# Kernel tuning notes

Measured on AMD Instinct MI355X. Metric: run time of the kernel, lower is better.

The kernel has to match this reference:

```python
import jax, jax.numpy as jnp
import numpy as np

N_NODES = 50000
N_EDGES = 800000


def _sage_layer(h, src, dst, ew, Ws, Wn, b, activate):
    # DGL SAGEConv, aggregator_type='mean', with edge weights:
    # message m_e = ew_e * h_src ; neigh = mean over incoming edges (divide by in-degree)
    msg = h[src] * ew[:, None]                       # [E, F] irregular gather
    agg = jax.ops.segment_sum(msg, dst, num_segments=N_NODES)
    deg = jax.ops.segment_sum(jnp.ones_like(ew), dst, num_segments=N_NODES)
    h_neigh = agg / jnp.maximum(deg, 1.0)[:, None]   # zero for isolated nodes
    out = h @ Ws + h_neigh @ Wn + b                  # fc_self + fc_neigh + bias
    return jnp.tanh(out) if activate else out


def setup_inputs() -> dict:
    key = jax.random.key(0)
    ks = jax.random.split(key, 12)
    d = 64
    inp = {
        "b_z": jax.random.normal(ks[0], (N_NODES, d), dtype=jnp.float32),
        "edge_src": jax.random.randint(ks[1], (N_EDGES,), 0, N_NODES, dtype=jnp.int32),
        "edge_dst": jax.random.randint(ks[2], (N_EDGES,), 0, N_NODES, dtype=jnp.int32),
        "edge_weight": jax.random.uniform(ks[3], (N_EDGES,), dtype=jnp.float32),
        "Ws0": jax.random.normal(ks[4], (64, 32), dtype=jnp.float32) / np.sqrt(64),
        "Wn0": jax.random.normal(ks[5], (64, 32), dtype=jnp.float32) / np.sqrt(64),
        "b0": jnp.zeros((32,), jnp.float32),
        "Ws1": jax.random.normal(ks[6], (32, 16), dtype=jnp.float32) / np.sqrt(32),
        "Wn1": jax.random.normal(ks[7], (32, 16), dtype=jnp.float32) / np.sqrt(32),
        "b1": jnp.zeros((16,), jnp.float32),
        "Ws2": jax.random.normal(ks[8], (16, 1), dtype=jnp.float32) / np.sqrt(16),
        "Wn2": jax.random.normal(ks[9], (16, 1), dtype=jnp.float32) / np.sqrt(16),
        "b2": jnp.zeros((1,), jnp.float32),
        "b_size": 500,
    }
    return inp


def reference(b_z, edge_src, edge_dst, edge_weight,
              Ws0, Wn0, b0, Ws1, Wn1, b1, Ws2, Wn2, b2, b_size):
    h = _sage_layer(b_z, edge_src, edge_dst, edge_weight, Ws0, Wn0, b0, True)
    h = _sage_layer(h, edge_src, edge_dst, edge_weight, Ws1, Wn1, b1, True)
    h = _sage_layer(h, edge_src, edge_dst, edge_weight, Ws2, Wn2, b2, False)
    x_hat = h.reshape(b_size, -1)
    return x_hat
```

## Files before the change

### kernel.cpp

```cpp
#include <hip/hip_runtime.h>
#include <hip/hip_bf16.h>

#define N_NODES 50000
#define N_EDGES 800000
#define BLK 256
#define NRANGE 256
#define RNG 196
#define NPART 256
#define EPB 3125
#define PCAP 44
#define SCAP 48
#define GRID_F 2048

#define EW_SCALE (1.0f / 65535.0f)

__device__ inline void unpack8(uint4 g, float* f) {
    f[0] = __uint_as_float(g.x << 16); f[1] = __uint_as_float(g.x & 0xffff0000u);
    f[2] = __uint_as_float(g.y << 16); f[3] = __uint_as_float(g.y & 0xffff0000u);
    f[4] = __uint_as_float(g.z << 16); f[5] = __uint_as_float(g.z & 0xffff0000u);
    f[6] = __uint_as_float(g.w << 16); f[7] = __uint_as_float(g.w & 0xffff0000u);
}
__device__ inline void unpack4(uint2 g, float* f) {
    f[0] = __uint_as_float(g.x << 16); f[1] = __uint_as_float(g.x & 0xffff0000u);
    f[2] = __uint_as_float(g.y << 16); f[3] = __uint_as_float(g.y & 0xffff0000u);
}

__global__ void premul0_partA_kernel(const float* __restrict__ b_z,
                                     const int* __restrict__ src,
                                     const int* __restrict__ dst,
                                     const float* __restrict__ ew,
                                     const float* __restrict__ Wn0,
                                     const float* __restrict__ Ws0,
                                     const float* __restrict__ b0,
                                     __hip_bfloat16* __restrict__ hW0,
                                     float* __restrict__ hSelf0,
                                     uint2* __restrict__ lists,
                                     int* __restrict__ pcnt, int N) {
    __shared__ __align__(16) unsigned char SMEM[28080];
    int tid = threadIdx.x;
    int bid = blockIdx.x;

    if (bid < NPART) {
        uint2* sSorted = (uint2*)SMEM;
        int* hist = (int*)(SMEM + 25000);
        int* pfx  = (int*)(SMEM + 26024);
        int* cur  = (int*)(SMEM + 27048);
        int base = bid * EPB;
        hist[tid] = 0;
        __syncthreads();
        for (int i = tid; i < EPB; i += BLK)
            atomicAdd(&hist[dst[base + i] / RNG], 1);
        __syncthreads();
        {
            int v = hist[tid];
            pfx[tid] = v;
            __syncthreads();
            for (int off = 1; off < NRANGE; off <<= 1) {
                int t = (tid >= off) ? pfx[tid - off] : 0;
                __syncthreads();
                pfx[tid] += t;
                __syncthreads();
            }
            int incl = pfx[tid];
            __syncthreads();
            pfx[tid] = incl - v;
            cur[tid] = incl - v;
            __syncthreads();
        }
        for (int i = tid; i < EPB; i += BLK) {
            int e = base + i;
            int d = dst[e];
            unsigned int q = __float2uint_rn(ew[e] * 65535.0f);
            unsigned int py = (q << 16) | (unsigned int)src[e];
            int pos = atomicAdd(&cur[d / RNG], 1);
            sSorted[pos] = make_uint2(py, (unsigned int)d);
        }
        __syncthreads();
        for (int i = tid; i < EPB; i += BLK) {
            int lo = 0, hi = NRANGE - 1;
            while (lo < hi) { int mid = (lo + hi + 1) >> 1; if (pfx[mid] <= i) lo = mid; else hi = mid - 1; }
            int idx = i - pfx[lo];
            if (idx < PCAP)
                lists[((size_t)lo * NPART + bid) * PCAP + idx] = sSorted[i];
        }
        pcnt[tid * NPART + bid] = min(hist[tid], PCAP);
    } else {
        float* sWn = (float*)SMEM;
        float* sWs = (float*)(SMEM + 8192);
        float* sb  = (float*)(SMEM + 16384);
        float* sh  = (float*)(SMEM + 16512);
        for (int i = tid; i < 64 * 32; i += BLK) { sWn[i] = Wn0[i]; sWs[i] = Ws0[i]; }
        if (tid < 32) sb[tid] = b0[tid];
        const int nch = (N + 7) / 8;
        const int stride = GRID_F - NPART;
        int r = tid >> 5, j = tid & 31;
        for (int c = bid - NPART; c < nch; c += stride) {
            __syncthreads();
            int nodeBase = c * 8;
            for (int i = tid; i < 8 * 64; i += BLK) {
                int rr = i >> 6, k = i & 63;
                int n = nodeBase + rr;
                sh[rr * 65 + k] = (n < N) ? b_z[(size_t)n * 64 + k] : 0.f;
            }
            __syncthreads();
            int n = nodeBase + r;
            if (n < N) {
                float an = 0.f, as = 0.f;
#pragma unroll
                for (int k = 0; k < 64; ++k) {
                    float hk = sh[r * 65 + k];
                    an += hk * sWn[k * 32 + j];
                    as += hk * sWs[k * 32 + j];
                }
                hW0[(size_t)n * 32 + j] = __float2bfloat16(an);
                hSelf0[(size_t)n * 32 + j] = as + sb[j];
            }
        }
    }
}

__global__ void partB_kernel(const uint2* __restrict__ lists,
                             const int* __restrict__ pcnt,
                             unsigned int* __restrict__ bucket,
                             int* __restrict__ counts, int N) {
    __shared__ unsigned int lslot[RNG * SCAP];
    __shared__ int lcnt[RNG];
    __shared__ int scnt[NPART];
    __shared__ int spfx[NPART];
    int tid = threadIdx.x;
    int r = blockIdx.x;
    int node0 = r * RNG;
    int nn = min(RNG, N - node0);
    if (nn <= 0) return;

    for (int i = tid; i < RNG; i += BLK) lcnt[i] = 0;
    scnt[tid] = pcnt[r * NPART + tid];
    __syncthreads();
    {
        int v = scnt[tid];
        spfx[tid] = v;
        __syncthreads();
        for (int off = 1; off < NPART; off <<= 1) {
            int t = (tid >= off) ? spfx[tid - off] : 0;
            __syncthreads();
            spfx[tid] += t;
            __syncthreads();
        }
        int incl = spfx[tid];
        __syncthreads();
        spfx[tid] = incl - v;
        __syncthreads();
    }
    int T = spfx[NPART - 1] + scnt[NPART - 1];
    for (int j = tid; j < T; j += BLK) {
        int lo = 0, hi = NPART - 1;
        while (lo < hi) { int mid = (lo + hi + 1) >> 1; if (spfx[mid] <= j) lo = mid; else hi = mid - 1; }
        int idx = j - spfx[lo];
        uint2 en = lists[((size_t)r * NPART + lo) * PCAP + idx];
        int node = (int)en.y - node0;
        int pos = atomicAdd(&lcnt[node], 1);
        if (pos < SCAP) lslot[node * SCAP + pos] = en.x;
    }
    __syncthreads();
    unsigned int* __restrict__ gb = bucket + (size_t)node0 * SCAP;
    int tot = nn * SCAP;
    for (int i = tid; i < tot; i += BLK) gb[i] = lslot[i];
    for (int i = tid; i < nn; i += BLK) counts[node0 + i] = min(lcnt[i], SCAP);
}

__global__ void agg0_kernel(const __hip_bfloat16* __restrict__ hW0,
                            const float* __restrict__ hSelf0,
                            const int* __restrict__ cnts,
                            const unsigned int* __restrict__ bucket,
                            const float* __restrict__ Wn1,
                            const float* __restrict__ Ws1,
                            const float* __restrict__ b1,
                            __hip_bfloat16* __restrict__ hW1,
                            float* __restrict__ hSelf1, int N) {
    __shared__ float sWn[32 * 16];
    __shared__ float sWs[32 * 16];
    __shared__ float sb[16];
    __shared__ float sh2[64 * 33];
    int tid = threadIdx.x;
    for (int i = tid; i < 32 * 16; i += BLK) { sWn[i] = Wn1[i]; sWs[i] = Ws1[i]; }
    if (tid < 16) sb[tid] = b1[tid];

    const uint4* __restrict__ tab = (const uint4*)hW0;
    int nodeBase = blockIdx.x * 64;
    int r = tid >> 2;
    int l = tid & 3;
    int n = nodeBase + r;
    if (n < N) {
        int cnt = cnts[n];
        int cn  = min(cnt, SCAP);
        const unsigned int* __restrict__ ep = bucket + (size_t)n * SCAP;
        float acc[8];
#pragma unroll
        for (int t = 0; t < 8; ++t) acc[t] = 0.f;
        int k = 0;
        for (; k + 8 <= cn; k += 8) {
            uint4 ev0 = *(const uint4*)(ep + k);
            uint4 ev1 = *(const uint4*)(ep + k + 4);
            unsigned int ee[8] = { ev0.x, ev0.y, ev0.z, ev0.w,
                                   ev1.x, ev1.y, ev1.z, ev1.w };
            uint4 g[8];
            float w[8];
#pragma unroll
            for (int u = 0; u < 8; ++u) {
                g[u] = tab[(size_t)(ee[u] & 0xffffu) * 4 + l];
                w[u] = (float)(ee[u] >> 16) * EW_SCALE;
            }
#pragma unroll
            for (int u = 0; u < 8; ++u) {
                float f[8];
                unpack8(g[u], f);
#pragma unroll
                for (int t = 0; t < 8; ++t) acc[t] += w[u] * f[t];
            }
        }
        for (; k < cn; ++k) {
            unsigned int e = ep[k];
            float w = (float)(e >> 16) * EW_SCALE;
            uint4 g = tab[(size_t)(e & 0xffffu) * 4 + l];
            float f[8];
            unpack8(g, f);
#pragma unroll
            for (int t = 0; t < 8; ++t) acc[t] += w * f[t];
        }
        float invdeg = 1.0f / fmaxf((float)cnt, 1.0f);
        const float4* __restrict__ hs = (const float4*)(hSelf0 + (size_t)n * 32);
        float4 s0 = hs[l * 2], s1 = hs[l * 2 + 1];
        float sf[8] = { s0.x, s0.y, s0.z, s0.w, s1.x, s1.y, s1.z, s1.w };
#pragma unroll
        for (int t = 0; t < 8; ++t)
            sh2[r * 33 + l * 8 + t] = tanhf(acc[t] * invdeg + sf[t]);
    }
    __syncthreads();
    for (int idx = tid; idx < 64 * 16; idx += BLK) {
        int r2 = idx >> 4, j2 = idx & 15;
        int n2 = nodeBase + r2;
        if (n2 < N) {
            float an = 0.f, as = 0.f;
#pragma unroll
            for (int k = 0; k < 32; ++k) {
                float hk = sh2[r2 * 33 + k];
                an += hk * sWn[k * 16 + j2];
                as += hk * sWs[k * 16 + j2];
            }
            hW1[(size_t)n2 * 16 + j2] = __float2bfloat16(an);
            hSelf1[(size_t)n2 * 16 + j2] = as + sb[j2];
        }
    }
}

__global__ void agg1_kernel(const __hip_bfloat16* __restrict__ hW1,
                            const float* __restrict__ hSelf1,
                            const int* __restrict__ cnts,
                            const unsigned int* __restrict__ bucket,
                            const float* __restrict__ Wn2,
                            const float* __restrict__ Ws2,
                            const float* __restrict__ b2,
                            float* __restrict__ hWf,
                            float* __restrict__ hSelf2, int N) {
    int tid = threadIdx.x;
    int r = tid >> 2;
    int l = tid & 3;
    int n = blockIdx.x * 64 + r;
    if (n >= N) return;

    const uint2* __restrict__ tab = (const uint2*)hW1;
    int cnt = cnts[n];
    int cn  = min(cnt, SCAP);
    const unsigned int* __restrict__ ep = bucket + (size_t)n * SCAP;
    float acc[4];
#pragma unroll
    for (int t = 0; t < 4; ++t) acc[t] = 0.f;
    int k = 0;
    for (; k + 8 <= cn; k += 8) {
        uint4 ev0 = *(const uint4*)(ep + k);
        uint4 ev1 = *(const uint4*)(ep + k + 4);
        unsigned int ee[8] = { ev0.x, ev0.y, ev0.z, ev0.w,
                               ev1.x, ev1.y, ev1.z, ev1.w };
        uint2 g[8];
        float w[8];
#pragma unroll
        for (int u = 0; u < 8; ++u) {
            g[u] = tab[(size_t)(ee[u] & 0xffffu) * 4 + l];
            w[u] = (float)(ee[u] >> 16) * EW_SCALE;
        }
#pragma unroll
        for (int u = 0; u < 8; ++u) {
            float f[4];
            unpack4(g[u], f);
#pragma unroll
            for (int t = 0; t < 4; ++t) acc[t] += w[u] * f[t];
        }
    }
    for (; k < cn; ++k) {
        unsigned int e = ep[k];
        float w = (float)(e >> 16) * EW_SCALE;
        uint2 g = tab[(size_t)(e & 0xffffu) * 4 + l];
        float f[4];
        unpack4(g, f);
#pragma unroll
        for (int t = 0; t < 4; ++t) acc[t] += w * f[t];
    }
    float invdeg = 1.0f / fmaxf((float)cnt, 1.0f);
    const float4* __restrict__ hs = (const float4*)(hSelf1 + (size_t)n * 16);
    float4 sv = hs[l];
    float sf[4] = { sv.x, sv.y, sv.z, sv.w };
    float t2 = 0.f, t3 = 0.f;
#pragma unroll
    for (int t = 0; t < 4; ++t) {
        float hv = tanhf(acc[t] * invdeg + sf[t]);
        t2 += hv * Wn2[l * 4 + t];
        t3 += hv * Ws2[l * 4 + t];
    }
    t2 += __shfl_xor(t2, 1, 4); t2 += __shfl_xor(t2, 2, 4);
    t3 += __shfl_xor(t3, 1, 4); t3 += __shfl_xor(t3, 2, 4);
    if (l == 0) {
        hWf[n] = t2;
        hSelf2[n] = t3 + b2[0];
    }
}

__global__ void agg_final_kernel(const float* __restrict__ hWf,
                                 const float* __restrict__ hSelf2,
                                 const int* __restrict__ cnts,
                                 const unsigned int* __restrict__ bucket,
                                 float* __restrict__ out, int N) {
    int sub = threadIdx.x & 15;
    int r   = threadIdx.x >> 4;
    int n   = blockIdx.x * 16 + r;
    if (n >= N) return;
    int cnt = cnts[n];
    int cn  = min(cnt, SCAP);
    const unsigned int* __restrict__ ep = bucket + (size_t)n * SCAP;
    float a = 0.f;
    for (int k = sub; k < cn; k += 16) {
        unsigned int e = ep[k];
        a += ((float)(e >> 16) * EW_SCALE) * hWf[e & 0xffffu];
    }
#pragma unroll
    for (int m = 8; m >= 1; m >>= 1) a += __shfl_xor(a, m, 16);
    if (sub == 0) {
        float invdeg = 1.0f / fmaxf((float)cnt, 1.0f);
        out[n] = a * invdeg + hSelf2[n];
    }
}

extern "C" void kernel_launch(void* const* d_in, const int* in_sizes, int n_in,
                              void* d_out, int out_size, void* d_ws, size_t ws_size,
                              hipStream_t stream) {
    const float* b_z = (const float*)d_in[0];
    const int*   src = (const int*)d_in[1];
    const int*   dst = (const int*)d_in[2];
    const float* ew  = (const float*)d_in[3];
    const float* Ws0 = (const float*)d_in[4];
    const float* Wn0 = (const float*)d_in[5];
    const float* b0  = (const float*)d_in[6];
    const float* Ws1 = (const float*)d_in[7];
    const float* Wn1 = (const float*)d_in[8];
    const float* b1  = (const float*)d_in[9];
    const float* Ws2 = (const float*)d_in[10];
    const float* Wn2 = (const float*)d_in[11];
    const float* b2  = (const float*)d_in[12];

    const int N = N_NODES;

    uint2*        lists  = (uint2*)d_ws;
    int*          pcnt   = (int*)(lists + (size_t)NRANGE * NPART * PCAP);
    int*          counts = pcnt + NRANGE * NPART;
    unsigned int* bucket = (unsigned int*)(counts + N);
    __hip_bfloat16* hW0  = (__hip_bfloat16*)(bucket + (size_t)N * SCAP);
    __hip_bfloat16* hW1  = hW0 + (size_t)N * 32;
    float* hWf    = (float*)(hW1 + (size_t)N * 16);
    float* hSelf0 = hWf + N;
    float* hSelf1 = hSelf0 + (size_t)N * 32;
    float* hSelf2 = hSelf1 + (size_t)N * 16;
    float* outp   = (float*)d_out;

    premul0_partA_kernel<<<GRID_F, BLK, 0, stream>>>(
        b_z, src, dst, ew, Wn0, Ws0, b0, hW0, hSelf0, lists, pcnt, N);
    partB_kernel<<<NRANGE, BLK, 0, stream>>>(lists, pcnt, bucket, counts, N);
    agg0_kernel<<<(N + 63) / 64, BLK, 0, stream>>>(
        hW0, hSelf0, counts, bucket, Wn1, Ws1, b1, hW1, hSelf1, N);
    agg1_kernel<<<(N + 63) / 64, BLK, 0, stream>>>(
        hW1, hSelf1, counts, bucket, Wn2, Ws2, b2, hWf, hSelf2, N);
    agg_final_kernel<<<(N + 15) / 16, BLK, 0, stream>>>(
        hWf, hSelf2, counts, bucket, outp, N);
}
```

Baseline: 89.32 us.

## Split layer-0 premultiply across partition stages to overlap with bucketing

The dense layer-0 premultiply (b_z times Wn0/Ws0) is factored into a device function and its node chunks are split into two halves. The first half runs alongside the edge partitioning pass and the second half alongside the per-range bucket fill, which was previously a 256-block kernel that left much of the GPU idle. The goal is to hide the second-stage latency behind useful dense work. In exchange the second stage now uses a larger 2048-block grid, and its shared-memory buffer grows to about 40 KB, which may lower occupancy for the premultiply blocks.

```diff
diff --git a/kernel.cpp b/kernel.cpp
--- a/kernel.cpp
+++ b/kernel.cpp
@@ -25,17 +25,57 @@
     f[2] = __uint_as_float(g.y << 16); f[3] = __uint_as_float(g.y & 0xffff0000u);
 }
 
-__global__ void premul0_partA_kernel(const float* __restrict__ b_z,
-                                     const int* __restrict__ src,
-                                     const int* __restrict__ dst,
-                                     const float* __restrict__ ew,
-                                     const float* __restrict__ Wn0,
-                                     const float* __restrict__ Ws0,
-                                     const float* __restrict__ b0,
-                                     __hip_bfloat16* __restrict__ hW0,
-                                     float* __restrict__ hSelf0,
-                                     uint2* __restrict__ lists,
-                                     int* __restrict__ pcnt, int N) {
+__device__ void premul0_work(unsigned char* SMEM,
+                             const float* __restrict__ b_z,
+                             const float* __restrict__ Wn0,
+                             const float* __restrict__ Ws0,
+                             const float* __restrict__ b0,
+                             __hip_bfloat16* __restrict__ hW0,
+                             float* __restrict__ hSelf0,
+                             int c0, int c1, int cstep, int cfirst, int N) {
+    int tid = threadIdx.x;
+    float* sWn = (float*)SMEM;
+    float* sWs = (float*)(SMEM + 8192);
+    float* sb  = (float*)(SMEM + 16384);
+    float* sh  = (float*)(SMEM + 16512);
+    for (int i = tid; i < 64 * 32; i += BLK) { sWn[i] = Wn0[i]; sWs[i] = Ws0[i]; }
+    if (tid < 32) sb[tid] = b0[tid];
+    int r = tid >> 5, j = tid & 31;
+    for (int c = c0 + cfirst; c < c1; c += cstep) {
+        __syncthreads();
+        int nodeBase = c * 8;
+        for (int i = tid; i < 8 * 64; i += BLK) {
+            int rr = i >> 6, k = i & 63;
+            int n = nodeBase + rr;
+            sh[rr * 65 + k] = (n < N) ? b_z[(size_t)n * 64 + k] : 0.f;
+        }
+        __syncthreads();
+        int n = nodeBase + r;
+        if (n < N) {
+            float an = 0.f, as = 0.f;
+#pragma unroll
+            for (int k = 0; k < 64; ++k) {
+                float hk = sh[r * 65 + k];
+                an += hk * sWn[k * 32 + j];
+                as += hk * sWs[k * 32 + j];
+            }
+            hW0[(size_t)n * 32 + j] = __float2bfloat16(an);
+            hSelf0[(size_t)n * 32 + j] = as + sb[j];
+        }
+    }
+}
+
+__global__ void stage1_kernel(const float* __restrict__ b_z,
+                              const int* __restrict__ src,
+                              const int* __restrict__ dst,
+                              const float* __restrict__ ew,
+                              const float* __restrict__ Wn0,
+                              const float* __restrict__ Ws0,
+                              const float* __restrict__ b0,
+                              __hip_bfloat16* __restrict__ hW0,
+                              float* __restrict__ hSelf0,
+                              uint2* __restrict__ lists,
+                              int* __restrict__ pcnt, int N) {
     __shared__ __align__(16) unsigned char SMEM[28080];
     int tid = threadIdx.x;
     int bid = blockIdx.x;
@@ -85,87 +125,71 @@
         }
         pcnt[tid * NPART + bid] = min(hist[tid], PCAP);
     } else {
-        float* sWn = (float*)SMEM;
-        float* sWs = (float*)(SMEM + 8192);
-        float* sb  = (float*)(SMEM + 16384);
-        float* sh  = (float*)(SMEM + 16512);
-        for (int i = tid; i < 64 * 32; i += BLK) { sWn[i] = Wn0[i]; sWs[i] = Ws0[i]; }
-        if (tid < 32) sb[tid] = b0[tid];
-        const int nch = (N + 7) / 8;
-        const int stride = GRID_F - NPART;
-        int r = tid >> 5, j = tid & 31;
-        for (int c = bid - NPART; c < nch; c += stride) {
+        premul0_work(SMEM, b_z, Wn0, Ws0, b0, hW0, hSelf0,
+                     0, 3125, GRID_F - NPART, bid - NPART, N);
+    }
+}
+
+__global__ void stage2_kernel(const float* __restrict__ b_z,
+                              const float* __restrict__ Wn0,
+                              const float* __restrict__ Ws0,
+                              const float* __restrict__ b0,
+                              __hip_bfloat16* __restrict__ hW0,
+                              float* __restrict__ hSelf0,
+                              const uint2* __restrict__ lists,
+                              const int* __restrict__ pcnt,
+                              unsigned int* __restrict__ bucket,
+                              int* __restrict__ counts, int N) {
+    __shared__ __align__(16) unsigned char SMEM[40464];
+    int tid = threadIdx.x;
+    int bid = blockIdx.x;
+
+    if (bid < NRANGE) {
+        unsigned int* lslot = (unsigned int*)SMEM;
+        int* lcnt = (int*)(SMEM + 37632);
+        int* scnt = (int*)(SMEM + 38416);
+        int* spfx = (int*)(SMEM + 39440);
+        int node0 = bid * RNG;
+        int nn = min(RNG, N - node0);
+        if (nn > 0) {
+            for (int i = tid; i < RNG; i += BLK) lcnt[i] = 0;
+            scnt[tid] = pcnt[bid * NPART + tid];
             __syncthreads();
-            int nodeBase = c * 8;
-            for (int i = tid; i < 8 * 64; i += BLK) {
-                int rr = i >> 6, k = i & 63;
-                int n = nodeBase + rr;
-                sh[rr * 65 + k] = (n < N) ? b_z[(size_t)n * 64 + k] : 0.f;
+            {
+                int v = scnt[tid];
+                spfx[tid] = v;
+                __syncthreads();
+                for (int off = 1; off < NPART; off <<= 1) {
+                    int t = (tid >= off) ? spfx[tid - off] : 0;
+                    __syncthreads();
+                    spfx[tid] += t;
+                    __syncthreads();
+                }
+                int incl = spfx[tid];
+                __syncthreads();
+                spfx[tid] = incl - v;
+                __syncthreads();
+            }
+            int T = spfx[NPART - 1] + scnt[NPART - 1];
+            for (int j = tid; j < T; j += BLK) {
+                int lo = 0, hi = NPART - 1;
+                while (lo < hi) { int mid = (lo + hi + 1) >> 1; if (spfx[mid] <= j) lo = mid; else hi = mid - 1; }
+                int idx = j - spfx[lo];
+                uint2 en = lists[((size_t)bid * NPART + lo) * PCAP + idx];
+                int node = (int)en.y - node0;
+                int pos = atomicAdd(&lcnt[node], 1);
+                if (pos < SCAP) lslot[node * SCAP + pos] = en.x;
             }
             __syncthreads();
-            int n = nodeBase + r;
-            if (n < N) {
-                float an = 0.f, as = 0.f;
-#pragma unroll
-                for (int k = 0; k < 64; ++k) {
-                    float hk = sh[r * 65 + k];
-                    an += hk * sWn[k * 32 + j];
-                    as += hk * sWs[k * 32 + j];
-                }
-                hW0[(size_t)n * 32 + j] = __float2bfloat16(an);
-                hSelf0[(size_t)n * 32 + j] = as + sb[j];
-            }
-        }
-    }
-}
-
-__global__ void partB_kernel(const uint2* __restrict__ lists,
-                             const int* __restrict__ pcnt,
-                             unsigned int* __restrict__ bucket,
-                             int* __restrict__ counts, int N) {
-    __shared__ unsigned int lslot[RNG * SCAP];
-    __shared__ int lcnt[RNG];
-    __shared__ int scnt[NPART];
-    __shared__ int spfx[NPART];
-    int tid = threadIdx.x;
-    int r = blockIdx.x;
-    int node0 = r * RNG;
-    int nn = min(RNG, N - node0);
-    if (nn <= 0) return;
-
-    for (int i = tid; i < RNG; i += BLK) lcnt[i] = 0;
-    scnt[tid] = pcnt[r * NPART + tid];
-    __syncthreads();
-    {
-        int v = scnt[tid];
-        spfx[tid] = v;
-        __syncthreads();
-        for (int off = 1; off < NPART; off <<= 1) {
-            int t = (tid >= off) ? spfx[tid - off] : 0;
-            __syncthreads();
-            spfx[tid] += t;
-            __syncthreads();
-        }
-        int incl = spfx[tid];
-        __syncthreads();
-        spfx[tid] = incl - v;
-        __syncthreads();
-    }
-    int T = spfx[NPART - 1] + scnt[NPART - 1];
-    for (int j = tid; j < T; j += BLK) {
-        int lo = 0, hi = NPART - 1;
-        while (lo < hi) { int mid = (lo + hi + 1) >> 1; if (spfx[mid] <= j) lo = mid; else hi = mid - 1; }
-        int idx = j - spfx[lo];
-        uint2 en = lists[((size_t)r * NPART + lo) * PCAP + idx];
-        int node = (int)en.y - node0;
-        int pos = atomicAdd(&lcnt[node], 1);
-        if (pos < SCAP) lslot[node * SCAP + pos] = en.x;
-    }
-    __syncthreads();
-    unsigned int* __restrict__ gb = bucket + (size_t)node0 * SCAP;
-    int tot = nn * SCAP;
-    for (int i = tid; i < tot; i += BLK) gb[i] = lslot[i];
-    for (int i = tid; i < nn; i += BLK) counts[node0 + i] = min(lcnt[i], SCAP);
+            unsigned int* gb = bucket + (size_t)node0 * SCAP;
+            int tot = nn * SCAP;
+            for (int i = tid; i < tot; i += BLK) gb[i] = lslot[i];
+            for (int i = tid; i < nn; i += BLK) counts[node0 + i] = min(lcnt[i], SCAP);
+        }
+    } else {
+        premul0_work(SMEM, b_z, Wn0, Ws0, b0, hW0, hSelf0,
+                     3125, 6250, GRID_F - NPART, bid - NPART, N);
+    }
 }
 
 __global__ void agg0_kernel(const __hip_bfloat16* __restrict__ hW0,
@@ -380,9 +404,10 @@
     float* hSelf2 = hSelf1 + (size_t)N * 16;
     float* outp   = (float*)d_out;
 
-    premul0_partA_kernel<<<GRID_F, BLK, 0, stream>>>(
+    stage1_kernel<<<GRID_F, BLK, 0, stream>>>(
         b_z, src, dst, ew, Wn0, Ws0, b0, hW0, hSelf0, lists, pcnt, N);
-    partB_kernel<<<NRANGE, BLK, 0, stream>>>(lists, pcnt, bucket, counts, N);
+    stage2_kernel<<<GRID_F, BLK, 0, stream>>>(
+        b_z, Wn0, Ws0, b0, hW0, hSelf0, lists, pcnt, bucket, counts, N);
     agg0_kernel<<<(N + 63) / 64, BLK, 0, stream>>>(
         hW0, hSelf0, counts, bucket, Wn1, Ws1, b1, hW1, hSelf1, N);
     agg1_kernel<<<(N + 63) / 64, BLK, 0, stream>>>(
```

New measurement: 291.8 us. +226.7%, slower.
